# Optimization experiments

Measured on AMD Instinct MI355X. Metric: run time of the kernel, lower is better.

Reference implementation:

```python
import math
import jax, jax.numpy as jnp
import numpy as np

B, S, D, H = 2, 2048, 768, 12
DK = D // H

def setup_inputs() -> dict:
    key = jax.random.key(0)
    ks = jax.random.split(key, 8)
    scale = 1.0 / math.sqrt(D)
    return {
        "Q": jax.random.normal(ks[0], (B, S, D), dtype=jnp.float32),
        "K": jax.random.normal(ks[1], (B, S, D), dtype=jnp.float32),
        "V": jax.random.normal(ks[2], (B, S, D), dtype=jnp.float32),
        "mask": jax.random.randint(ks[3], (B, 1, S, S), 0, 2, dtype=jnp.int32),
        "W_Q": jax.random.normal(ks[4], (D, D), dtype=jnp.float32) * scale,
        "W_K": jax.random.normal(ks[5], (D, D), dtype=jnp.float32) * scale,
        "W_V": jax.random.normal(ks[6], (D, D), dtype=jnp.float32) * scale,
        "W_O": jax.random.normal(ks[7], (D, D), dtype=jnp.float32) * scale,
    }

def reference(Q, K, V, mask, W_Q, W_K, W_V, W_O):
    # torch Linear: y = x @ W.T (weight shape [out, in], no bias)
    q = (Q @ W_Q.T).reshape(B, S, H, DK).transpose(0, 2, 1, 3)  # [B,H,S,dk]
    k = (K @ W_K.T).reshape(B, S, H, DK).transpose(0, 2, 1, 3)
    v = (V @ W_V.T).reshape(B, S, H, DK).transpose(0, 2, 1, 3)
    scores = jnp.einsum('bhqd,bhkd->bhqk', q, k) / math.sqrt(DK)
    scores = jnp.where(mask == 0, -jnp.inf, scores)
    weights = jax.nn.softmax(scores, axis=-1)
    weights = jnp.nan_to_num(weights, nan=0.0)
    out = jnp.einsum('bhqk,bhkd->bhqd', weights, v)  # [B,H,S,dk]
    out = out.transpose(0, 2, 1, 3).reshape(B, S, D)
    return out @ W_O.T
```

## Files before the change

### kernel.cpp

```cpp
#include <hip/hip_runtime.h>
#include <hip/hip_bf16.h>
#include <stdint.h>

typedef __attribute__((ext_vector_type(8))) short bf16x8;
typedef __attribute__((ext_vector_type(4))) short bf16x4;
typedef __attribute__((ext_vector_type(4))) float f32x4;
typedef __attribute__((ext_vector_type(16))) float f32x16;
typedef __attribute__((ext_vector_type(4))) unsigned short u16x4;

__device__ __forceinline__ unsigned short f2bf(float x) {
  union { __hip_bfloat16 h; unsigned short s; } u;
  u.h = __float2bfloat16(x);
  return u.s;
}
__device__ __forceinline__ unsigned int cvtpk(float lo, float hi) {
  unsigned int r;
  asm("v_cvt_pk_bf16_f32 %0, %1, %2" : "=v"(r) : "v"(lo), "v"(hi));
  return r;
}
__device__ __forceinline__ void gll16(const unsigned short* g, unsigned short* l) {
  __builtin_amdgcn_global_load_lds(
      (const __attribute__((address_space(1))) unsigned int*)g,
      (__attribute__((address_space(3))) unsigned int*)l, 16, 0, 0);
}

__global__ __launch_bounds__(256) void prep_kernel(
    const int* __restrict__ mask, unsigned int* __restrict__ mp,
    const float* __restrict__ q, const float* __restrict__ k, const float* __restrict__ v,
    const float* __restrict__ wq, const float* __restrict__ wk, const float* __restrict__ wv,
    const float* __restrict__ wo,
    unsigned short* __restrict__ qb, unsigned short* __restrict__ kb, unsigned short* __restrict__ vb,
    unsigned short* __restrict__ wqb, unsigned short* __restrict__ wkb,
    unsigned short* __restrict__ wvb, unsigned short* __restrict__ wob) {
  if (blockIdx.x < 1024) {
    const int widx = blockIdx.x * 256 + threadIdx.x;
    const int* src = mask + (size_t)widx * 32;
    unsigned int wbits = 0;
#pragma unroll
    for (int j = 0; j < 8; ++j) {
      int4 vv = *(const int4*)(src + j * 4);
      wbits |= (vv.x != 0 ? 1u : 0u) << (j * 4 + 0);
      wbits |= (vv.y != 0 ? 1u : 0u) << (j * 4 + 1);
      wbits |= (vv.z != 0 ? 1u : 0u) << (j * 4 + 2);
      wbits |= (vv.w != 0 ? 1u : 0u) << (j * 4 + 3);
    }
    mp[widx] = wbits;
  } else {
    const int U = 1474560;
    const int stride = 2880 * 256;
    for (int u = (blockIdx.x - 1024) * 256 + threadIdx.x; u < U; u += stride) {
      const float* s; unsigned short* d; int r; float scale = 1.0f;
      if (u < 1179648) {
        int which = u / 393216; r = u - which * 393216;
        s = (which == 0) ? q : (which == 1) ? k : v;
        d = (which == 0) ? qb : (which == 1) ? kb : vb;
      } else {
        int u2 = u - 1179648; int which = u2 / 73728; r = u2 - which * 73728;
        s = (which == 0) ? wq : (which == 1) ? wk : (which == 2) ? wv : wo;
        d = (which == 0) ? wqb : (which == 1) ? wkb : (which == 2) ? wvb : wob;
        if (which == 0) scale = 0.18033688f;
      }
      float4 a = *(const float4*)&s[(size_t)r * 8];
      float4 b2 = *(const float4*)&s[(size_t)r * 8 + 4];
      uint4 o;
      o.x = cvtpk(a.x * scale, a.y * scale);
      o.y = cvtpk(a.z * scale, a.w * scale);
      o.z = cvtpk(b2.x * scale, b2.y * scale);
      o.w = cvtpk(b2.z * scale, b2.w * scale);
      *(uint4*)&d[(size_t)r * 8] = o;
    }
  }
}

__global__ __launch_bounds__(256) void maskpack_kernel(const int* __restrict__ mask,
                                                       unsigned int* __restrict__ mp,
                                                       int total) {
  int i = blockIdx.x * blockDim.x + threadIdx.x;
  const int lane = threadIdx.x & 63;
  const int stride = gridDim.x * blockDim.x;
  for (; i < total; i += stride) {
    unsigned long long b = __ballot(mask[i] != 0);
    if (lane == 0)       mp[i >> 5] = (unsigned int)b;
    else if (lane == 32) mp[i >> 5] = (unsigned int)(b >> 32);
  }
}

#define GEMM_BODY(AEXPR, BEXPR)                                                   \
  __shared__ unsigned short As[3][128][32];                                       \
  __shared__ unsigned short Bs[3][128][32];                                       \
  const int m0 = blockIdx.y * 128, n0 = blockIdx.x * 128;                         \
  const int t = threadIdx.x, lane = t & 63, w = t >> 6;                           \
  const int wr = w >> 1, wc = w & 1, fr = lane & 15, cl = lane >> 4;              \
  const int srl = lane >> 2, sph = lane & 3;                                      \
  f32x4 acc[4][4] = {};                                                           \
  auto ISSUE = [&](int kk, int buf) {                                             \
    _Pragma("unroll")                                                             \
    for (int i = 0; i < 2; ++i) {                                                 \
      const int row = i * 64 + w * 16 + srl;                                      \
      const int c = sph ^ ((row >> 1) & 3);                                       \
      gll16(AEXPR, &As[buf][i * 64 + w * 16][0]);                                 \
      gll16(BEXPR, &Bs[buf][i * 64 + w * 16][0]);                                 \
    }                                                                             \
  };                                                                              \
  ISSUE(0, 0);                                                                    \
  ISSUE(32, 1);                                                                   \
  asm volatile("s_waitcnt vmcnt(4)" ::: "memory");                                \
  __syncthreads();                                                                \
  for (int it = 0; it < 24; ++it) {                                               \
    const int buf = it - (it / 3) * 3;                                            \
    if (it < 22) {                                                                \
      const int nb = (it + 2) - ((it + 2) / 3) * 3;                               \
      ISSUE((it + 2) * 32, nb);                                                   \
    }                                                                             \
    bf16x8 af[4], bfr[4];                                                         \
    _Pragma("unroll")                                                             \
    for (int i = 0; i < 4; ++i) {                                                 \
      const int R = wr * 64 + i * 16 + fr;                                        \
      af[i] = *(const bf16x8*)&As[buf][R][(cl ^ ((R >> 1) & 3)) * 8];             \
    }                                                                             \
    _Pragma("unroll")                                                             \
    for (int j = 0; j < 4; ++j) {                                                 \
      const int R = wc * 64 + j * 16 + fr;                                        \
      bfr[j] = *(const bf16x8*)&Bs[buf][R][(cl ^ ((R >> 1) & 3)) * 8];            \
    }                                                                             \
    __builtin_amdgcn_s_setprio(1);                                                \
    _Pragma("unroll")                                                             \
    for (int i = 0; i < 4; ++i)                                                   \
      _Pragma("unroll")                                                           \
      for (int j = 0; j < 4; ++j)                                                 \
        acc[i][j] = __builtin_amdgcn_mfma_f32_16x16x32_bf16(af[i], bfr[j],        \
                                                            acc[i][j], 0, 0, 0); \
    __builtin_amdgcn_s_setprio(0);                                                \
    if (it < 22) asm volatile("s_waitcnt vmcnt(4)" ::: "memory");                 \
    else         asm volatile("s_waitcnt vmcnt(0)" ::: "memory");                 \
    __syncthreads();                                                              \
  }

__global__ __launch_bounds__(256) void proj_b16(
    const unsigned short* __restrict__ Qb, const unsigned short* __restrict__ Kb,
    const unsigned short* __restrict__ Vb,
    const unsigned short* __restrict__ Wqb, const unsigned short* __restrict__ Wkb,
    const unsigned short* __restrict__ Wvb,
    unsigned short* __restrict__ qo, unsigned short* __restrict__ ko,
    unsigned short* __restrict__ vo) {
  const int z = blockIdx.z;
  const unsigned short* A = (z == 0) ? Qb : (z == 1) ? Kb : Vb;
  const unsigned short* W = (z == 0) ? Wqb : (z == 1) ? Wkb : Wvb;
  GEMM_BODY(A + (size_t)(m0 + row) * 768 + kk + c * 8,
            W + (size_t)(n0 + row) * 768 + kk + c * 8)
  if (z == 2) {
    for (int i = 0; i < 4; ++i)
      for (int j = 0; j < 4; ++j) {
        int m = m0 + wr * 64 + i * 16 + (lane >> 4) * 4;
        int n = n0 + wc * 64 + j * 16 + fr;
        int b = m >> 11, s = m & 2047, hd = n >> 6, dk = n & 63;
        u16x4 pk;
        for (int r = 0; r < 4; ++r) pk[r] = f2bf(acc[i][j][r]);
        *(u16x4*)&vo[((size_t)(b * 12 + hd) * 64 + dk) * 2048 + s] = pk;
      }
  } else {
    unsigned short* O = (z == 0) ? qo : ko;
    for (int i = 0; i < 4; ++i)
      for (int j = 0; j < 4; ++j)
        for (int r = 0; r < 4; ++r) {
          int m = m0 + wr * 64 + i * 16 + (lane >> 4) * 4 + r;
          int n = n0 + wc * 64 + j * 16 + fr;
          int b = m >> 11, s = m & 2047, hd = n >> 6, dk = n & 63;
          O[((size_t)(b * 12 + hd) * 2048 + s) * 64 + dk] = f2bf(acc[i][j][r]);
        }
  }
}

__global__ __launch_bounds__(256) void out_b16(
    const unsigned short* __restrict__ Ain, const unsigned short* __restrict__ Wob,
    float* __restrict__ Out) {
  GEMM_BODY(Ain + (size_t)(m0 + row) * 768 + kk + c * 8,
            Wob + (size_t)(n0 + row) * 768 + kk + c * 8)
  for (int i = 0; i < 4; ++i)
    for (int j = 0; j < 4; ++j)
      for (int r = 0; r < 4; ++r) {
        int m = m0 + wr * 64 + i * 16 + (lane >> 4) * 4 + r;
        int n = n0 + wc * 64 + j * 16 + fr;
        Out[(size_t)m * 768 + n] = acc[i][j][r];
      }
}

__global__ __launch_bounds__(256) void proj_gemm(
    const float* __restrict__ Qi, const float* __restrict__ Ki, const float* __restrict__ Vi,
    const float* __restrict__ Wq, const float* __restrict__ Wk, const float* __restrict__ Wv,
    unsigned short* __restrict__ qo, unsigned short* __restrict__ ko, unsigned short* __restrict__ vo) {
  constexpr int LDT = 56;
  __shared__ unsigned short As[128][LDT];
  __shared__ unsigned short Bs[128][LDT];
  const int z = blockIdx.z;
  const float* A = (z == 0) ? Qi : (z == 1) ? Ki : Vi;
  const float* W = (z == 0) ? Wq : (z == 1) ? Wk : Wv;
  const int m0 = blockIdx.y * 128, n0 = blockIdx.x * 128;
  const int t = threadIdx.x, lane = t & 63, w = t >> 6;
  const int wr = w >> 1, wc = w & 1;
  const int fr = lane & 15, fg = (lane >> 4) * 8;
  const int srow = t >> 3, sseg = t & 7;
  f32x4 acc[4][4] = {};
  for (int kk = 0; kk < 768; kk += 32) {
    for (int pp = 0; pp < 4; ++pp) {
      int row = srow + pp * 32;
      float4 fa = *(const float4*)&A[(size_t)(m0 + row) * 768 + kk + sseg * 4];
      float4 fb = *(const float4*)&W[(size_t)(n0 + row) * 768 + kk + sseg * 4];
      bf16x4 pa = {(short)f2bf(fa.x), (short)f2bf(fa.y), (short)f2bf(fa.z), (short)f2bf(fa.w)};
      bf16x4 pb = {(short)f2bf(fb.x), (short)f2bf(fb.y), (short)f2bf(fb.z), (short)f2bf(fb.w)};
      *(bf16x4*)&As[row][sseg * 4] = pa;
      *(bf16x4*)&Bs[row][sseg * 4] = pb;
    }
    __syncthreads();
    bf16x8 af[4], bfr[4];
    for (int i = 0; i < 4; ++i) af[i]  = *(const bf16x8*)&As[wr * 64 + i * 16 + fr][fg];
    for (int i = 0; i < 4; ++i) bfr[i] = *(const bf16x8*)&Bs[wc * 64 + i * 16 + fr][fg];
    for (int i = 0; i < 4; ++i)
      for (int j = 0; j < 4; ++j)
        acc[i][j] = __builtin_amdgcn_mfma_f32_16x16x32_bf16(af[i], bfr[j], acc[i][j], 0, 0, 0);
    __syncthreads();
  }
  if (z == 2) {
    for (int i = 0; i < 4; ++i)
      for (int j = 0; j < 4; ++j) {
        int m = m0 + wr * 64 + i * 16 + (lane >> 4) * 4;
        int n = n0 + wc * 64 + j * 16 + fr;
        int b = m >> 11, s = m & 2047, hd = n >> 6, dk = n & 63;
        u16x4 pk;
        for (int r = 0; r < 4; ++r) pk[r] = f2bf(acc[i][j][r]);
        *(u16x4*)&vo[((size_t)(b * 12 + hd) * 64 + dk) * 2048 + s] = pk;
      }
  } else {
    unsigned short* O = (z == 0) ? qo : ko;
    const float scale = (z == 0) ? 0.18033688f : 1.0f;
    for (int i = 0; i < 4; ++i)
      for (int j = 0; j < 4; ++j)
        for (int r = 0; r < 4; ++r) {
          int m = m0 + wr * 64 + i * 16 + (lane >> 4) * 4 + r;
          int n = n0 + wc * 64 + j * 16 + fr;
          int b = m >> 11, s = m & 2047, hd = n >> 6, dk = n & 63;
          O[((size_t)(b * 12 + hd) * 2048 + s) * 64 + dk] = f2bf(acc[i][j][r] * scale);
        }
  }
}

__global__ __launch_bounds__(256) void out_gemm(
    const unsigned short* __restrict__ Ain, const float* __restrict__ W,
    float* __restrict__ Out) {
  constexpr int LDT = 56;
  __shared__ unsigned short As[128][LDT];
  __shared__ unsigned short Bs[128][LDT];
  const int m0 = blockIdx.y * 128, n0 = blockIdx.x * 128;
  const int t = threadIdx.x, lane = t & 63, w = t >> 6;
  const int wr = w >> 1, wc = w & 1;
  const int fr = lane & 15, fg = (lane >> 4) * 8;
  f32x4 acc[4][4] = {};
  for (int kk = 0; kk < 768; kk += 32) {
    {
      int row = t >> 2, seg = t & 3;
      for (int pp = 0; pp < 2; ++pp) {
        bf16x8 va = *(const bf16x8*)&Ain[(size_t)(m0 + row + pp * 64) * 768 + kk + seg * 8];
        *(bf16x8*)&As[row + pp * 64][seg * 8] = va;
      }
      int row2 = t >> 3, seg2 = t & 7;
      for (int pp = 0; pp < 4; ++pp) {
        float4 fb = *(const float4*)&W[(size_t)(n0 + row2 + pp * 32) * 768 + kk + seg2 * 4];
        bf16x4 pb = {(short)f2bf(fb.x), (short)f2bf(fb.y), (short)f2bf(fb.z), (short)f2bf(fb.w)};
        *(bf16x4*)&Bs[row2 + pp * 32][seg2 * 4] = pb;
      }
    }
    __syncthreads();
    bf16x8 af[4], bfr[4];
    for (int i = 0; i < 4; ++i) af[i]  = *(const bf16x8*)&As[wr * 64 + i * 16 + fr][fg];
    for (int i = 0; i < 4; ++i) bfr[i] = *(const bf16x8*)&Bs[wc * 64 + i * 16 + fr][fg];
    for (int i = 0; i < 4; ++i)
      for (int j = 0; j < 4; ++j)
        acc[i][j] = __builtin_amdgcn_mfma_f32_16x16x32_bf16(af[i], bfr[j], acc[i][j], 0, 0, 0);
    __syncthreads();
  }
  for (int i = 0; i < 4; ++i)
    for (int j = 0; j < 4; ++j)
      for (int r = 0; r < 4; ++r) {
        int m = m0 + wr * 64 + i * 16 + (lane >> 4) * 4 + r;
        int n = n0 + wc * 64 + j * 16 + fr;
        Out[(size_t)m * 768 + n] = acc[i][j][r];
      }
}

__global__ __launch_bounds__(1024) void attn16_kernel(
    const unsigned short* __restrict__ qh, const unsigned short* __restrict__ kh,
    const unsigned short* __restrict__ vh, const unsigned int* __restrict__ mp,
    unsigned short* __restrict__ ao) {
  __shared__ union LdsU {
    struct {
      unsigned short K[2][4][32][64];
      unsigned short V[2][4][64][32];
    } st;
    float M16[16][16][64];
  } lds;
  __shared__ float Sm[16][64];
  __shared__ float Sl[16][64];
  const int t = threadIdx.x, lane = t & 63, w = t >> 6;
  const int wq = w & 3, sp = w >> 2;
  const int bid = blockIdx.x;
  const int xcd = bid & 7, idx = bid >> 3;
  const int bh = xcd * 3 + (idx >> 4);
  const int qb = idx & 15;
  const int bb = bh / 12, hh = bh % 12;
  const int qc = lane & 31, h = lane >> 5;
  const int q = qb * 128 + wq * 32 + qc;
  const unsigned short* qrow = qh + ((size_t)bh * 2048 + q) * 64;
  bf16x8 bq[4];
#pragma unroll
  for (int kc = 0; kc < 4; ++kc) bq[kc] = *(const bf16x8*)(qrow + kc * 16 + h * 8);
  const unsigned int* mrow = mp + ((size_t)bb * 2048 + q) * 64 + sp * 16;
  const unsigned short* kgb = kh + (size_t)bh * 2048 * 64;
  const unsigned short* vgb = vh + (size_t)bh * 64 * 2048;
  f32x16 acc0 = {}, acc1 = {};
  float l_run = 0.f;
  float m_run = -1e30f;
  const int KT0 = sp * 512;
  const int krow = lane >> 3, ksch = (lane & 7) ^ (lane >> 3);
  const int vrow = lane >> 2, vsch = (lane & 3) ^ ((lane >> 3) & 3);
  auto ISSUE = [&](int it2, int b2) {
    const int KT = KT0 + it2 * 32;
    unsigned short* kd = &lds.st.K[b2][sp][0][0];
    unsigned short* vd = &lds.st.V[b2][sp][0][0];
    const int c = wq;
    gll16(kgb + (size_t)(KT + c * 8 + krow) * 64 + ksch * 8, kd + c * 512);
    gll16(vgb + (size_t)(c * 16 + vrow) * 2048 + KT + vsch * 8, vd + c * 512);
  };
  ISSUE(0, 0);
#pragma unroll 2
  for (int it = 0; it < 16; ++it) {
    const int b = it & 1;
    asm volatile("s_waitcnt vmcnt(0)" ::: "memory");
    __syncthreads();
    if (it < 15) ISSUE(it + 1, b ^ 1);
    const unsigned int m32 = mrow[it];
    bf16x8 ka[4];
#pragma unroll
    for (int kc = 0; kc < 4; ++kc)
      ka[kc] = *(const bf16x8*)&lds.st.K[b][sp][qc][((kc * 2 + h) ^ (qc & 7)) * 8];
    f32x16 sc = {};
    __builtin_amdgcn_s_setprio(1);
#pragma unroll
    for (int kc = 0; kc < 4; ++kc)
      sc = __builtin_amdgcn_mfma_f32_32x32x16_bf16(ka[kc], bq[kc], sc, 0, 0, 0);
    __builtin_amdgcn_s_setprio(0);
    bf16x8 va0[2], va1[2];
#pragma unroll
    for (int ks = 0; ks < 2; ++ks) {
      const int cs = ((ks * 2 + h) ^ ((qc >> 1) & 3)) * 8;
      va0[ks] = *(const bf16x8*)&lds.st.V[b][sp][qc][cs];
      va1[ks] = *(const bf16x8*)&lds.st.V[b][sp][32 + qc][cs];
    }
    const unsigned int wsh = m32 >> (4 * h);
#pragma unroll
    for (int r = 0; r < 16; ++r) {
      const int sh = (r & 3) + 8 * (r >> 2);
      sc[r] = ((wsh >> sh) & 1u) ? sc[r] : -3.0e38f;
    }
    float mA0 = fmaxf(fmaxf(sc[0], sc[4]), fmaxf(sc[8], sc[12]));
    float mA1 = fmaxf(fmaxf(sc[1], sc[5]), fmaxf(sc[9], sc[13]));
    float mA2 = fmaxf(fmaxf(sc[2], sc[6]), fmaxf(sc[10], sc[14]));
    float mA3 = fmaxf(fmaxf(sc[3], sc[7]), fmaxf(sc[11], sc[15]));
    float m1 = fmaxf(fmaxf(mA0, mA1), fmaxf(mA2, mA3));
    float tmax = fmaxf(m1, __shfl_xor(m1, 32, 64));
    if (__any(tmax > m_run + 8.0f)) {
      float mnew = fmaxf(m_run, tmax);
      float scl = exp2f(m_run - mnew);
      m_run = mnew;
      l_run *= scl;
#pragma unroll
      for (int e = 0; e < 16; ++e) { acc0[e] *= scl; acc1[e] *= scl; }
    }
#pragma unroll
    for (int r = 0; r < 16; ++r) sc[r] = exp2f(sc[r] - m_run);
    float sA0 = (sc[0] + sc[4]) + (sc[8] + sc[12]);
    float sA1 = (sc[1] + sc[5]) + (sc[9] + sc[13]);
    float sA2 = (sc[2] + sc[6]) + (sc[10] + sc[14]);
    float sA3 = (sc[3] + sc[7]) + (sc[11] + sc[15]);
    float s1 = (sA0 + sA1) + (sA2 + sA3);
    l_run += s1 + __shfl_xor(s1, 32, 64);
    __builtin_amdgcn_s_setprio(1);
#define PVQ(P, OFF, A0, A1) { \
    unsigned int a0 = cvtpk(P[OFF + 0], P[OFF + 1]), a1 = cvtpk(P[OFF + 2], P[OFF + 3]); \
    unsigned int b0 = cvtpk(P[OFF + 4], P[OFF + 5]), b1 = cvtpk(P[OFF + 6], P[OFF + 7]); \
    asm("v_permlane32_swap_b32 %0, %1" : "+v"(a0), "+v"(b0)); \
    asm("v_permlane32_swap_b32 %0, %1" : "+v"(a1), "+v"(b1)); \
    union { unsigned int u[4]; bf16x8 v; } bfu; \
    bfu.u[0] = a0; bfu.u[1] = a1; bfu.u[2] = b0; bfu.u[3] = b1; \
    acc0 = __builtin_amdgcn_mfma_f32_32x32x16_bf16(A0, bfu.v, acc0, 0, 0, 0); \
    acc1 = __builtin_amdgcn_mfma_f32_32x32x16_bf16(A1, bfu.v, acc1, 0, 0, 0); }
    PVQ(sc, 0, va0[0], va1[0]);
    PVQ(sc, 8, va0[1], va1[1]);
#undef PVQ
    __builtin_amdgcn_s_setprio(0);
  }
  __syncthreads();
  Sm[w][lane] = m_run;
  Sl[w][lane] = l_run;
#pragma unroll
  for (int e = 0; e < 16; ++e) lds.M16[w][e][lane] = acc0[e];
  __syncthreads();
  float pm0 = Sm[wq][lane],     pm1 = Sm[4 + wq][lane];
  float pm2 = Sm[8 + wq][lane], pm3 = Sm[12 + wq][lane];
  float M = fmaxf(fmaxf(pm0, pm1), fmaxf(pm2, pm3));
  float w0 = exp2f(pm0 - M), w1 = exp2f(pm1 - M), w2 = exp2f(pm2 - M), w3 = exp2f(pm3 - M);
  float L = Sl[wq][lane] * w0 + Sl[4 + wq][lane] * w1 +
            Sl[8 + wq][lane] * w2 + Sl[12 + wq][lane] * w3;
  float inv = (L > 0.f) ? 1.0f / L : 0.f;
  unsigned short* orow = ao + ((size_t)bb * 2048 + q) * 768 + hh * 64;
  if (sp < 2) {
    const int e0 = sp * 8;
#pragma unroll
    for (int g = 0; g < 2; ++g) {
      u16x4 pk4;
#pragma unroll
      for (int j = 0; j < 4; ++j) {
        const int e = e0 + g * 4 + j;
        float v = (lds.M16[wq][e][lane] * w0 + lds.M16[4 + wq][e][lane] * w1 +
                   lds.M16[8 + wq][e][lane] * w2 + lds.M16[12 + wq][e][lane] * w3) * inv;
        pk4[j] = f2bf(v);
      }
      const int d0 = 8 * ((e0 + g * 4) >> 2) + 4 * h;
      *(u16x4*)&orow[d0] = pk4;
    }
  }
  __syncthreads();
#pragma unroll
  for (int e = 0; e < 16; ++e) lds.M16[w][e][lane] = acc1[e];
  __syncthreads();
  if (sp >= 2) {
    const int e0 = (sp - 2) * 8;
#pragma unroll
    for (int g = 0; g < 2; ++g) {
      u16x4 pk4;
#pragma unroll
      for (int j = 0; j < 4; ++j) {
        const int e = e0 + g * 4 + j;
        float v = (lds.M16[wq][e][lane] * w0 + lds.M16[4 + wq][e][lane] * w1 +
                   lds.M16[8 + wq][e][lane] * w2 + lds.M16[12 + wq][e][lane] * w3) * inv;
        pk4[j] = f2bf(v);
      }
      const int d0 = 32 + 8 * ((e0 + g * 4) >> 2) + 4 * h;
      *(u16x4*)&orow[d0] = pk4;
    }
  }
}

__global__ __launch_bounds__(512) void attn_kernel(
    const unsigned short* __restrict__ qh, const unsigned short* __restrict__ kh,
    const unsigned short* __restrict__ vh, const unsigned int* __restrict__ mp,
    unsigned short* __restrict__ ao) {
  __shared__ union LdsU {
    struct {
      unsigned short K[2][4][32][64];
      unsigned short V[2][4][64][32];
    } st;
    float M[8][32][64];
  } lds;
  __shared__ float Sm[8][64];
  __shared__ float Sl[8][64];
  const int t = threadIdx.x, lane = t & 63, w = t >> 6;
  const int wq = w & 1, sp = w >> 1;
  const int bid = blockIdx.x;
  const int xcd = bid & 7, idx = bid >> 3;
  const int bh = xcd * 3 + (idx >> 5);
  const int qb = idx & 31;
  const int bb = bh / 12, hh = bh % 12;
  const int qc = lane & 31, h = lane >> 5;
  const int q = qb * 64 + wq * 32 + qc;
  const unsigned short* qrow = qh + ((size_t)bh * 2048 + q) * 64;
  bf16x8 bq[4];
#pragma unroll
  for (int kc = 0; kc < 4; ++kc) bq[kc] = *(const bf16x8*)(qrow + kc * 16 + h * 8);
  const unsigned int* mrow = mp + ((size_t)bb * 2048 + q) * 64 + sp * 16;
  const unsigned short* kgb = kh + (size_t)bh * 2048 * 64;
  const unsigned short* vgb = vh + (size_t)bh * 64 * 2048;
  f32x16 acc0 = {}, acc1 = {};
  float l_run = 0.f;
  float m_run = -1e30f;
  const int KT0 = sp * 512;
  const int krow = lane >> 3, ksch = (lane & 7) ^ (lane >> 3);
  const int vrow = lane >> 2, vsch = (lane & 3) ^ ((lane >> 3) & 3);
  auto ISSUE = [&](int it2, int b2) {
    const int KT = KT0 + it2 * 32;
    unsigned short* kd = &lds.st.K[b2][sp][0][0];
    unsigned short* vd = &lds.st.V[b2][sp][0][0];
#pragma unroll
    for (int c2 = 0; c2 < 2; ++c2) {
      const int c = 2 * wq + c2;
      gll16(kgb + (size_t)(KT + c * 8 + krow) * 64 + ksch * 8, kd + c * 512);
    }
#pragma unroll
    for (int c2 = 0; c2 < 2; ++c2) {
      const int c = 2 * wq + c2;
      gll16(vgb + (size_t)(c * 16 + vrow) * 2048 + KT + vsch * 8, vd + c * 512);
    }
  };
  ISSUE(0, 0);
#pragma unroll 2
  for (int it = 0; it < 16; ++it) {
    const int b = it & 1;
    asm volatile("s_waitcnt vmcnt(0)" ::: "memory");
    __syncthreads();
    if (it < 15) ISSUE(it + 1, b ^ 1);
    const unsigned int m32 = mrow[it];
    bf16x8 ka[4];
#pragma unroll
    for (int kc = 0; kc < 4; ++kc)
      ka[kc] = *(const bf16x8*)&lds.st.K[b][sp][qc][((kc * 2 + h) ^ (qc & 7)) * 8];
    f32x16 sc = {};
    __builtin_amdgcn_s_setprio(1);
#pragma unroll
    for (int kc = 0; kc < 4; ++kc)
      sc = __builtin_amdgcn_mfma_f32_32x32x16_bf16(ka[kc], bq[kc], sc, 0, 0, 0);
    __builtin_amdgcn_s_setprio(0);
    bf16x8 va0[2], va1[2];
#pragma unroll
    for (int ks = 0; ks < 2; ++ks) {
      const int cs = ((ks * 2 + h) ^ ((qc >> 1) & 3)) * 8;
      va0[ks] = *(const bf16x8*)&lds.st.V[b][sp][qc][cs];
      va1[ks] = *(const bf16x8*)&lds.st.V[b][sp][32 + qc][cs];
    }
    const unsigned int wsh = m32 >> (4 * h);
#pragma unroll
    for (int r = 0; r < 16; ++r) {
      const int sh = (r & 3) + 8 * (r >> 2);
      sc[r] = ((wsh >> sh) & 1u) ? sc[r] : -3.0e38f;
    }
    float mA0 = fmaxf(fmaxf(sc[0], sc[4]), fmaxf(sc[8], sc[12]));
    float mA1 = fmaxf(fmaxf(sc[1], sc[5]), fmaxf(sc[9], sc[13]));
    float mA2 = fmaxf(fmaxf(sc[2], sc[6]), fmaxf(sc[10], sc[14]));
    float mA3 = fmaxf(fmaxf(sc[3], sc[7]), fmaxf(sc[11], sc[15]));
    float m1 = fmaxf(fmaxf(mA0, mA1), fmaxf(mA2, mA3));
    float tmax = fmaxf(m1, __shfl_xor(m1, 32, 64));
    if (__any(tmax > m_run + 8.0f)) {
      float mnew = fmaxf(m_run, tmax);
      float scl = exp2f(m_run - mnew);
      m_run = mnew;
      l_run *= scl;
#pragma unroll
      for (int e = 0; e < 16; ++e) { acc0[e] *= scl; acc1[e] *= scl; }
    }
#pragma unroll
    for (int r = 0; r < 16; ++r) sc[r] = exp2f(sc[r] - m_run);
    float sA0 = (sc[0] + sc[4]) + (sc[8] + sc[12]);
    float sA1 = (sc[1] + sc[5]) + (sc[9] + sc[13]);
    float sA2 = (sc[2] + sc[6]) + (sc[10] + sc[14]);
    float sA3 = (sc[3] + sc[7]) + (sc[11] + sc[15]);
    float s1 = (sA0 + sA1) + (sA2 + sA3);
    l_run += s1 + __shfl_xor(s1, 32, 64);
    __builtin_amdgcn_s_setprio(1);
#define PVQ(P, OFF, A0, A1) { \
    unsigned int a0 = cvtpk(P[OFF + 0], P[OFF + 1]), a1 = cvtpk(P[OFF + 2], P[OFF + 3]); \
    unsigned int b0 = cvtpk(P[OFF + 4], P[OFF + 5]), b1 = cvtpk(P[OFF + 6], P[OFF + 7]); \
    asm("v_permlane32_swap_b32 %0, %1" : "+v"(a0), "+v"(b0)); \
    asm("v_permlane32_swap_b32 %0, %1" : "+v"(a1), "+v"(b1)); \
    union { unsigned int u[4]; bf16x8 v; } bfu; \
    bfu.u[0] = a0; bfu.u[1] = a1; bfu.u[2] = b0; bfu.u[3] = b1; \
    acc0 = __builtin_amdgcn_mfma_f32_32x32x16_bf16(A0, bfu.v, acc0, 0, 0, 0); \
    acc1 = __builtin_amdgcn_mfma_f32_32x32x16_bf16(A1, bfu.v, acc1, 0, 0, 0); }
    PVQ(sc, 0, va0[0], va1[0]);
    PVQ(sc, 8, va0[1], va1[1]);
#undef PVQ
    __builtin_amdgcn_s_setprio(0);
  }
  __syncthreads();
  Sm[w][lane] = m_run;
  Sl[w][lane] = l_run;
#pragma unroll
  for (int e = 0; e < 16; ++e) lds.M[w][e][lane] = acc0[e];
#pragma unroll
  for (int e = 0; e < 16; ++e) lds.M[w][16 + e][lane] = acc1[e];
  __syncthreads();
  float pm0 = Sm[wq][lane],     pm1 = Sm[2 + wq][lane];
  float pm2 = Sm[4 + wq][lane], pm3 = Sm[6 + wq][lane];
  float M = fmaxf(fmaxf(pm0, pm1), fmaxf(pm2, pm3));
  float w0 = exp2f(pm0 - M), w1 = exp2f(pm1 - M), w2 = exp2f(pm2 - M), w3 = exp2f(pm3 - M);
  float L = Sl[wq][lane] * w0 + Sl[2 + wq][lane] * w1 +
            Sl[4 + wq][lane] * w2 + Sl[6 + wq][lane] * w3;
  float inv = (L > 0.f) ? 1.0f / L : 0.f;
  unsigned short* orow = ao + ((size_t)bb * 2048 + q) * 768 + hh * 64;
#pragma unroll
  for (int g = 0; g < 2; ++g) {
    const int e0 = sp * 8 + g * 4;
    const int base = (e0 >= 16) ? 32 : 0;
    const int er0 = e0 & 15;
    const int d0 = base + 8 * (er0 >> 2) + 4 * h;
    u16x4 pk4;
#pragma unroll
    for (int j = 0; j < 4; ++j) {
      float v = (lds.M[wq][e0 + j][lane] * w0 + lds.M[2 + wq][e0 + j][lane] * w1 +
                 lds.M[4 + wq][e0 + j][lane] * w2 + lds.M[6 + wq][e0 + j][lane] * w3) * inv;
      pk4[j] = f2bf(v);
    }
    *(u16x4*)&orow[d0] = pk4;
  }
}

extern "C" void kernel_launch(void* const* d_in, const int* in_sizes, int n_in,
                              void* d_out, int out_size, void* d_ws, size_t ws_size,
                              hipStream_t stream) {
  const float* Q  = (const float*)d_in[0];
  const float* K  = (const float*)d_in[1];
  const float* V  = (const float*)d_in[2];
  const int*   mask = (const int*)d_in[3];
  const float* WQ = (const float*)d_in[4];
  const float* WK = (const float*)d_in[5];
  const float* WV = (const float*)d_in[6];
  const float* WO = (const float*)d_in[7];
  float* out = (float*)d_out;
  char* ws = (char*)d_ws;

  const size_t NEED = 43515904ull;
  if (ws_size >= NEED) {
    unsigned short* qh  = (unsigned short*)(ws + 0);
    unsigned short* kh  = (unsigned short*)(ws + 6291456);
    unsigned short* vh  = (unsigned short*)(ws + 12582912);
    unsigned int*   mp  = (unsigned int*)(ws + 18874368);
    unsigned short* Qb  = (unsigned short*)(ws + 19922944);
    unsigned short* ao  = Qb;
    unsigned short* Kb  = (unsigned short*)(ws + 26214400);
    unsigned short* Vb  = (unsigned short*)(ws + 32505856);
    unsigned short* Wqb = (unsigned short*)(ws + 38797312);
    unsigned short* Wkb = (unsigned short*)(ws + 39976960);
    unsigned short* Wvb = (unsigned short*)(ws + 41156608);
    unsigned short* Wob = (unsigned short*)(ws + 42336256);
    prep_kernel<<<dim3(3904), 256, 0, stream>>>(mask, mp, Q, K, V, WQ, WK, WV, WO,
                                                Qb, Kb, Vb, Wqb, Wkb, Wvb, Wob);
    proj_b16<<<dim3(6, 32, 3), 256, 0, stream>>>(Qb, Kb, Vb, Wqb, Wkb, Wvb, qh, kh, vh);
    attn16_kernel<<<dim3(384), 1024, 0, stream>>>(qh, kh, vh, mp, ao);
    out_b16<<<dim3(6, 32), 256, 0, stream>>>(ao, Wob, out);
  } else {
    unsigned short* qh = (unsigned short*)(ws + 0);
    unsigned short* kh = (unsigned short*)(ws + 6291456);
    unsigned short* vh = (unsigned short*)(ws + 12582912);
    unsigned short* ao = (unsigned short*)(ws + 18874368);
    unsigned int*   mp = (unsigned int*)(ws + 25165824);
    maskpack_kernel<<<dim3(2048), 256, 0, stream>>>(mask, mp, 2 * 2048 * 2048);
    proj_gemm<<<dim3(6, 32, 3), 256, 0, stream>>>(Q, K, V, WQ, WK, WV, qh, kh, vh);
    attn_kernel<<<dim3(768), 512, 0, stream>>>(qh, kh, vh, mp, ao);
    out_gemm<<<dim3(6, 32), 256, 0, stream>>>(ao, WO, out);
  }
}
```

Before: 169.3 us.

## Replace 16-wave attention block with 4-wave blocks splitting keys two ways

The attention kernel goes from 1024-thread blocks (4 query tiles by 4 key splits) to 256-thread blocks (2 query tiles by 2 key splits), launched as 768 blocks instead of 384. Each wave now walks 1024 keys instead of 512, and each wave issues two K and two V loads per stage. The merge step combines only two partial softmax states and writes all 32 accumulator rows at once, which removes one LDS round trip and one barrier. The aim is cheaper block-wide barriers and a lighter merge, at the cost of longer serial key loops per wave and less K/V reuse per block.

```diff
diff --git a/kernel.cpp b/kernel.cpp
--- a/kernel.cpp
+++ b/kernel.cpp
@@ -287,56 +287,63 @@
       }
 }
 
-__global__ __launch_bounds__(1024) void attn16_kernel(
+__global__ __launch_bounds__(256) void attn4_kernel(
     const unsigned short* __restrict__ qh, const unsigned short* __restrict__ kh,
     const unsigned short* __restrict__ vh, const unsigned int* __restrict__ mp,
     unsigned short* __restrict__ ao) {
   __shared__ union LdsU {
     struct {
-      unsigned short K[2][4][32][64];
-      unsigned short V[2][4][64][32];
+      unsigned short K[2][2][32][64];
+      unsigned short V[2][2][64][32];
     } st;
-    float M16[16][16][64];
+    float M[4][32][64];
   } lds;
-  __shared__ float Sm[16][64];
-  __shared__ float Sl[16][64];
+  __shared__ float Sm[4][64];
+  __shared__ float Sl[4][64];
   const int t = threadIdx.x, lane = t & 63, w = t >> 6;
-  const int wq = w & 3, sp = w >> 2;
+  const int wq = w & 1, sp = w >> 1;
   const int bid = blockIdx.x;
   const int xcd = bid & 7, idx = bid >> 3;
-  const int bh = xcd * 3 + (idx >> 4);
-  const int qb = idx & 15;
+  const int bh = xcd * 3 + (idx >> 5);
+  const int qb = idx & 31;
   const int bb = bh / 12, hh = bh % 12;
   const int qc = lane & 31, h = lane >> 5;
-  const int q = qb * 128 + wq * 32 + qc;
+  const int q = qb * 64 + wq * 32 + qc;
   const unsigned short* qrow = qh + ((size_t)bh * 2048 + q) * 64;
   bf16x8 bq[4];
 #pragma unroll
   for (int kc = 0; kc < 4; ++kc) bq[kc] = *(const bf16x8*)(qrow + kc * 16 + h * 8);
-  const unsigned int* mrow = mp + ((size_t)bb * 2048 + q) * 64 + sp * 16;
+  const unsigned int* mrow = mp + ((size_t)bb * 2048 + q) * 64 + sp * 32;
   const unsigned short* kgb = kh + (size_t)bh * 2048 * 64;
   const unsigned short* vgb = vh + (size_t)bh * 64 * 2048;
   f32x16 acc0 = {}, acc1 = {};
   float l_run = 0.f;
   float m_run = -1e30f;
-  const int KT0 = sp * 512;
+  const int KT0 = sp * 1024;
   const int krow = lane >> 3, ksch = (lane & 7) ^ (lane >> 3);
   const int vrow = lane >> 2, vsch = (lane & 3) ^ ((lane >> 3) & 3);
   auto ISSUE = [&](int it2, int b2) {
     const int KT = KT0 + it2 * 32;
     unsigned short* kd = &lds.st.K[b2][sp][0][0];
     unsigned short* vd = &lds.st.V[b2][sp][0][0];
-    const int c = wq;
-    gll16(kgb + (size_t)(KT + c * 8 + krow) * 64 + ksch * 8, kd + c * 512);
-    gll16(vgb + (size_t)(c * 16 + vrow) * 2048 + KT + vsch * 8, vd + c * 512);
+#pragma unroll
+    for (int c2 = 0; c2 < 2; ++c2) {
+      const int c = 2 * wq + c2;
+      gll16(kgb + (size_t)(KT + c * 8 + krow) * 64 + ksch * 8, kd + c * 512);
+    }
+#pragma unroll
+    for (int c2 = 0; c2 < 2; ++c2) {
+      const int c = 2 * wq + c2;
+      gll16(vgb + (size_t)(c * 16 + vrow) * 2048 + KT + vsch * 8, vd + c * 512);
+    }
   };
   ISSUE(0, 0);
 #pragma unroll 2
-  for (int it = 0; it < 16; ++it) {
+  for (int it = 0; it < 32; ++it) {
     const int b = it & 1;
     asm volatile("s_waitcnt vmcnt(0)" ::: "memory");
     __syncthreads();
-    if (it < 15) ISSUE(it + 1, b ^ 1);
+    if (it < 31) ISSUE(it + 1, b ^ 1);
     const unsigned int m32 = mrow[it];
     bf16x8 ka[4];
 #pragma unroll
@@ -402,51 +409,29 @@
   Sm[w][lane] = m_run;
   Sl[w][lane] = l_run;
 #pragma unroll
-  for (int e = 0; e < 16; ++e) lds.M16[w][e][lane] = acc0[e];
+  for (int e = 0; e < 16; ++e) lds.M[w][e][lane] = acc0[e];
+#pragma unroll
+  for (int e = 0; e < 16; ++e) lds.M[w][16 + e][lane] = acc1[e];
   __syncthreads();
-  float pm0 = Sm[wq][lane],     pm1 = Sm[4 + wq][lane];
-  float pm2 = Sm[8 + wq][lane], pm3 = Sm[12 + wq][lane];
-  float M = fmaxf(fmaxf(pm0, pm1), fmaxf(pm2, pm3));
-  float w0 = exp2f(pm0 - M), w1 = exp2f(pm1 - M), w2 = exp2f(pm2 - M), w3 = exp2f(pm3 - M);
-  float L = Sl[wq][lane] * w0 + Sl[4 + wq][lane] * w1 +
-            Sl[8 + wq][lane] * w2 + Sl[12 + wq][lane] * w3;
+  float pm0 = Sm[wq][lane], pm1 = Sm[2 + wq][lane];
+  float M = fmaxf(pm0, pm1);
+  float w0 = exp2f(pm0 - M), w1 = exp2f(pm1 - M);
+  float L = Sl[wq][lane] * w0 + Sl[2 + wq][lane] * w1;
   float inv = (L > 0.f) ? 1.0f / L : 0.f;
   unsigned short* orow = ao + ((size_t)bb * 2048 + q) * 768 + hh * 64;
-  if (sp < 2) {
-    const int e0 = sp * 8;
-#pragma unroll
-    for (int g = 0; g < 2; ++g) {
-      u16x4 pk4;
-#pragma unroll
-      for (int j = 0; j < 4; ++j) {
-        const int e = e0 + g * 4 + j;
-        float v = (lds.M16[wq][e][lane] * w0 + lds.M16[4 + wq][e][lane] * w1 +
-                   lds.M16[8 + wq][e][lane] * w2 + lds.M16[12 + wq][e][lane] * w3) * inv;
-        pk4[j] = f2bf(v);
-      }
-      const int d0 = 8 * ((e0 + g * 4) >> 2) + 4 * h;
-      *(u16x4*)&orow[d0] = pk4;
-    }
-  }
-  __syncthreads();
-#pragma unroll
-  for (int e = 0; e < 16; ++e) lds.M16[w][e][lane] = acc1[e];
-  __syncthreads();
-  if (sp >= 2) {
-    const int e0 = (sp - 2) * 8;
-#pragma unroll
-    for (int g = 0; g < 2; ++g) {
-      u16x4 pk4;
-#pragma unroll
-      for (int j = 0; j < 4; ++j) {
-        const int e = e0 + g * 4 + j;
-        float v = (lds.M16[wq][e][lane] * w0 + lds.M16[4 + wq][e][lane] * w1 +
-                   lds.M16[8 + wq][e][lane] * w2 + lds.M16[12 + wq][e][lane] * w3) * inv;
-        pk4[j] = f2bf(v);
-      }
-      const int d0 = 32 + 8 * ((e0 + g * 4) >> 2) + 4 * h;
-      *(u16x4*)&orow[d0] = pk4;
-    }
+#pragma unroll
+  for (int g = 0; g < 4; ++g) {
+    const int e0 = sp * 16 + g * 4;
+    const int base = (e0 >= 16) ? 32 : 0;
+    const int er0 = e0 & 15;
+    const int d0 = base + 8 * (er0 >> 2) + 4 * h;
+    u16x4 pk4;
+#pragma unroll
+    for (int j = 0; j < 4; ++j) {
+      float v = (lds.M[wq][e0 + j][lane] * w0 + lds.M[2 + wq][e0 + j][lane] * w1) * inv;
+      pk4[j] = f2bf(v);
+    }
+    *(u16x4*)&orow[d0] = pk4;
   }
 }
 
@@ -632,7 +617,7 @@
     prep_kernel<<<dim3(3904), 256, 0, stream>>>(mask, mp, Q, K, V, WQ, WK, WV, WO,
                                                 Qb, Kb, Vb, Wqb, Wkb, Wvb, Wob);
     proj_b16<<<dim3(6, 32, 3), 256, 0, stream>>>(Qb, Kb, Vb, Wqb, Wkb, Wvb, qh, kh, vh);
-    attn16_kernel<<<dim3(384), 1024, 0, stream>>>(qh, kh, vh, mp, ao);
+    attn4_kernel<<<dim3(768), 256, 0, stream>>>(qh, kh, vh, mp, ao);
     out_b16<<<dim3(6, 32), 256, 0, stream>>>(ao, Wob, out);
   } else {
     unsigned short* qh = (unsigned short*)(ws + 0);
```

After: 165.6 us. 2.2% less time.
